# Performance work log

Measured on AMD Instinct MI355X. Metric: run time of the kernel, lower is better.

The kernel has to match this reference:

```python
import jax, jax.numpy as jnp
import numpy as np

D_MODEL = 1024
N_HEADS = 16
D_HEAD = D_MODEL // N_HEADS
MAX_K_LEN = 1024
SYNTH_HIDDEN = 1024
B, TQ, TK = 2, 1024, 1024
CAUSAL = True


def setup_inputs() -> dict:
    key = jax.random.key(0)
    ks = jax.random.split(key, 12)
    s = 1.0 / np.sqrt(D_MODEL)
    inp = {
        "x_q": jax.random.normal(ks[0], (B, TQ, D_MODEL), jnp.float32),
        "x_kv": jax.random.normal(ks[1], (B, TK, D_MODEL), jnp.float32),
        "key_padding_mask": jnp.ones((B, TK), jnp.int32),
        # projection weights stored [in, out] (equivalent to torch Linear)
        "Wq": jax.random.normal(ks[2], (D_MODEL, D_MODEL), jnp.float32) * s,
        "bq": jnp.zeros((D_MODEL,), jnp.float32),
        "Wk": jax.random.normal(ks[3], (D_MODEL, D_MODEL), jnp.float32) * s,
        "bk": jnp.zeros((D_MODEL,), jnp.float32),
        "Wv": jax.random.normal(ks[4], (D_MODEL, D_MODEL), jnp.float32) * s,
        "bv": jnp.zeros((D_MODEL,), jnp.float32),
        "Wo": jax.random.normal(ks[5], (D_MODEL, D_MODEL), jnp.float32) * s,
        "bo": jnp.zeros((D_MODEL,), jnp.float32),
        # synthesizer MLP: d_model -> synth_hidden -> n_heads*max_k_len
        "Ws1": jax.random.normal(ks[6], (D_MODEL, SYNTH_HIDDEN), jnp.float32) * s,
        "bs1": jnp.zeros((SYNTH_HIDDEN,), jnp.float32),
        "Ws2": jax.random.normal(ks[7], (SYNTH_HIDDEN, N_HEADS * MAX_K_LEN), jnp.float32) * (1.0 / np.sqrt(SYNTH_HIDDEN)),
        "bs2": jnp.zeros((N_HEADS * MAX_K_LEN,), jnp.float32),
        # gate logits init at log(0.5/0.5) = 0 -> sigmoid = 0.5
        "gate": jnp.zeros((N_HEADS,), jnp.float32),
    }
    return inp


def _attention(x_q, x_kv, key_padding_mask, Wq, bq, Wk, bk, Wv, bv, Wo, bo,
               Ws1, bs1, Ws2, bs2, gate):
    B_, Tq, _ = x_q.shape
    Tk = x_kv.shape[1]
    scale = D_HEAD ** -0.5

    def shape_heads(x):  # [B,T,D] -> [B,H,T,dh]
        return x.reshape(B_, -1, N_HEADS, D_HEAD).transpose(0, 2, 1, 3)

    Q = shape_heads(x_q @ Wq + bq)
    K = shape_heads(x_kv @ Wk + bk)
    V = shape_heads(x_kv @ Wv + bv)

    vanilla = jnp.einsum("bhqd,bhkd->bhqk", Q, K) * scale

    # dense synthesizer: MLP(x_q) -> [B,Tq,H,max_k_len] -> [B,H,Tq,Tk]
    h = jax.nn.gelu(x_q @ Ws1 + bs1, approximate=False)
    S = (h @ Ws2 + bs2).reshape(B_, Tq, N_HEADS, MAX_K_LEN)
    synth = S.transpose(0, 2, 1, 3)[:, :, :, :Tk]

    g = jax.nn.sigmoid(gate).reshape(1, N_HEADS, 1, 1)
    logits = (1.0 - g) * vanilla + g * synth

    # key padding mask: 1 = keep, 0 = pad
    keep = (key_padding_mask > 0).reshape(B_, 1, 1, Tk)
    logits = jnp.where(keep, logits, -jnp.inf)
    if CAUSAL:
        causal_mask = jnp.tril(jnp.ones((Tq, Tk), bool))  # keep lower triangle
        logits = jnp.where(causal_mask, logits, -jnp.inf)

    attn = jax.nn.softmax(logits, axis=-1)
    ctx = jnp.einsum("bhqk,bhkd->bhqd", attn, V)
    out = ctx.transpose(0, 2, 1, 3).reshape(B_, Tq, D_MODEL)
    return out @ Wo + bo


def reference(x_q, x_kv, key_padding_mask, Wq, bq, Wk, bk, Wv, bv, Wo, bo,
              Ws1, bs1, Ws2, bs2, gate):
    return _attention(x_q, x_kv, key_padding_mask, Wq, bq, Wk, bk, Wv, bv,
                      Wo, bo, Ws1, bs1, Ws2, bs2, gate)
```

## Files before the change

kernel.cpp:

```cpp
#include <hip/hip_runtime.h>
#include <hip/hip_bf16.h>

#define D_MODEL 1024
#define N_HEADS 16
#define MAX_K_LEN 1024
#define B_SZ 2
#define TQ 1024
#define TK 1024
#define M_ROWS 2048
#define NKL 16384

using bf16x8 = __attribute__((ext_vector_type(8))) short;
using f32x4  = __attribute__((ext_vector_type(4))) float;
using u16x8  = __attribute__((ext_vector_type(8))) unsigned short;

__device__ __forceinline__ unsigned short f2b(float f) {
    unsigned u = __float_as_uint(f);
    u = (u + 0x7FFFu + ((u >> 16) & 1u)) >> 16;
    return (unsigned short)u;
}
__device__ __forceinline__ float b2f(unsigned short u) {
    return __uint_as_float(((unsigned)u) << 16);
}

__device__ __forceinline__ void async_cp16(void* lds, const void* g) {
    __builtin_amdgcn_global_load_lds(
        (__attribute__((address_space(1))) void*)(void*)g,
        (__attribute__((address_space(3))) void*)lds, 16, 0, 0);
}

__device__ __forceinline__ int xrow(int row) {
    return (row & 7) ^ (((row >> 3) & 3) << 1);
}

__device__ __forceinline__ void ptile128_core(
    const unsigned short* __restrict__ A, const unsigned short* __restrict__ Wt,
    const float* __restrict__ bias, unsigned short* __restrict__ C,
    int N, int m0g, int n0g, int act, const float* __restrict__ gate,
    unsigned short* lds)
{
    constexpr int NT = 32;
    const int tid = threadIdx.x;
    const int lane = tid & 63;
    const int fr = lane & 15, rg = lane >> 4;
    const int w = tid >> 6;
    const int wr = w >> 1, wc = w & 1;

    const int sr = tid >> 2;
    const int sc = ((tid & 3) ^ ((sr >> 1) & 3)) * 8;
    const unsigned short* gA = A  + (size_t)(m0g + sr) * 1024 + sc;
    const unsigned short* gB = Wt + (size_t)(n0g + sr) * 1024 + sc;

    auto stage = [&](int t) {
        unsigned short* bufA = lds + (t % 3) * 8192;
        unsigned short* bufB = bufA + 4096;
        const int k0 = t * 32;
        async_cp16(bufA + tid*8,        gA + k0);
        async_cp16(bufA + 2048 + tid*8, gA + (size_t)64*1024 + k0);
        async_cp16(bufB + tid*8,        gB + k0);
        async_cp16(bufB + 2048 + tid*8, gB + (size_t)64*1024 + k0);
    };

    f32x4 acc[4][4];
#pragma unroll
    for (int i = 0; i < 4; ++i)
#pragma unroll
        for (int j = 0; j < 4; ++j) { f32x4 z = {0.f,0.f,0.f,0.f}; acc[i][j] = z; }

    const int fko = (rg ^ ((fr >> 1) & 3)) * 8;

    stage(0); stage(1);
    asm volatile("s_waitcnt vmcnt(4)" ::: "memory");
    __builtin_amdgcn_s_barrier();
    __builtin_amdgcn_sched_barrier(0);

    for (int t = 0; t < NT; ++t) {
        const unsigned short* bufA = lds + (t % 3) * 8192;
        const unsigned short* bufB = bufA + 4096;

        bf16x8 afr[4], bfr[4];
#pragma unroll
        for (int mi = 0; mi < 4; ++mi)
            afr[mi] = *(const bf16x8*)(bufA + (wr*64 + mi*16 + fr)*32 + fko);
#pragma unroll
        for (int ni = 0; ni < 4; ++ni)
            bfr[ni] = *(const bf16x8*)(bufB + (wc*64 + ni*16 + fr)*32 + fko);
        if (t + 2 < NT) stage(t + 2);

        __builtin_amdgcn_s_setprio(1);
#pragma unroll
        for (int mi = 0; mi < 4; ++mi)
#pragma unroll
            for (int ni = 0; ni < 4; ++ni)
                acc[mi][ni] = __builtin_amdgcn_mfma_f32_16x16x32_bf16(
                    afr[mi], bfr[ni], acc[mi][ni], 0, 0, 0);
        __builtin_amdgcn_s_setprio(0);

        if (t < NT - 2)       asm volatile("s_waitcnt vmcnt(4)" ::: "memory");
        else if (t == NT - 2) asm volatile("s_waitcnt vmcnt(0)" ::: "memory");
        __builtin_amdgcn_s_barrier();
        __builtin_amdgcn_sched_barrier(0);
    }

    float qs = 1.f;
    if (act == 2) {
        const float gg = 1.f / (1.f + __expf(-gate[(n0g + wc*64) >> 6]));
        qs = (1.f - gg) * 0.125f;
    }

    unsigned short* scr = lds + w * 1024;
    float bv[4];
#pragma unroll
    for (int ni = 0; ni < 4; ++ni) bv[ni] = bias[n0g + wc*64 + ni*16 + fr];
    const int ro = lane >> 3;
    const int co = (lane & 7) * 8;
#pragma unroll
    for (int mi = 0; mi < 4; ++mi) {
#pragma unroll
        for (int ni = 0; ni < 4; ++ni)
#pragma unroll
            for (int r = 0; r < 4; ++r) {
                float c = acc[mi][ni][r] + bv[ni];
                if (act == 1) c = 0.5f * c * (1.f + erff(c * 0.70710678118654752f));
                else if (act == 2) c *= qs;
                scr[(rg*4 + r)*64 + ni*16 + fr] = f2b(c);
            }
#pragma unroll
        for (int p = 0; p < 2; ++p) {
            const int row = p*8 + ro;
            const u16x8 v = *(const u16x8*)(scr + row*64 + co);
            *(u16x8*)(C + (size_t)(m0g + wr*64 + mi*16 + row) * N + n0g + wc*64 + co) = v;
        }
    }
}

struct QkvhArgs {
    const unsigned short* A[4];
    const unsigned short* W[4];
    const float* bias[4];
    void* out[4];
    const float* gate;
};

__global__ __launch_bounds__(256, 3) void gemm_qkvh_p(QkvhArgs args) {
    __shared__ __align__(16) unsigned short lds[24576];
    const int z = blockIdx.z;
    const int m0 = (blockIdx.x >> 3) * 128;
    const int n0 = (blockIdx.x & 7) * 128;
    const int act = (z == 3) ? 1 : ((z == 0) ? 2 : 0);
    ptile128_core(args.A[z], args.W[z], args.bias[z],
                  (unsigned short*)args.out[z], D_MODEL, m0, n0, act, args.gate, lds);
}

__global__ __launch_bounds__(256, 3) void gemm_logits_p(
    const unsigned short* __restrict__ A, const unsigned short* __restrict__ Wt,
    const float* __restrict__ bias, unsigned short* __restrict__ C,
    const unsigned short* __restrict__ Qpre, const unsigned short* __restrict__ Kb,
    const int* __restrict__ kpm)
{
    __shared__ __align__(16) unsigned short lds[24576];
    constexpr int NT = 34;
    const int bid = blockIdx.x;
    const int xcd = bid & 7;
    const int i = bid >> 3;
    const int hi = (i >= 72) ? 1 : 0;
    const int head = xcd * 2 + hi;
    const int j = i - hi * 72;
    int kq, idx;
    if (j < 16)      { kq = 0; idx = j; }
    else if (j < 30) { kq = 1; idx = j - 16; }
    else if (j < 42) { kq = 2; idx = j - 30; }
    else if (j < 52) { kq = 3; idx = j - 42; }
    else if (j < 60) { kq = 4; idx = j - 52; }
    else if (j < 66) { kq = 5; idx = j - 60; }
    else if (j < 70) { kq = 6; idx = j - 66; }
    else             { kq = 7; idx = j - 70; }
    const int b = idx & 1;
    const int rq = kq + (idx >> 1);
    const int m0g = (b * 8 + rq) * 128;
    const int n0g = (head * 8 + kq) * 128;

    const int tid = threadIdx.x;
    const int lane = tid & 63;
    const int fr = lane & 15, rg = lane >> 4;
    const int w = tid >> 6;
    const int wr = w >> 1, wc = w & 1;

    const int sr = tid >> 2;
    const int sc = ((tid & 3) ^ ((sr >> 1) & 3)) * 8;
    const unsigned short* gA = A  + (size_t)(m0g + sr) * 1024 + sc;
    const unsigned short* gB = Wt + (size_t)(n0g + sr) * 1024 + sc;
    const int q0 = rq * 128, k0a = kq * 128;
    const unsigned short* gA2 = Qpre + (size_t)(b*TQ + q0 + sr) * 1024 + head*64 + sc;
    const unsigned short* gB2 = Kb   + (size_t)(b*TK + k0a + sr) * 1024 + head*64 + sc;

    auto stageQK = [&](int t) {
        unsigned short* bufA = lds + (t % 3) * 8192;
        unsigned short* bufB = bufA + 4096;
        const int k0 = t * 32;
        async_cp16(bufA + tid*8,        gA2 + k0);
        async_cp16(bufA + 2048 + tid*8, gA2 + (size_t)64*1024 + k0);
        async_cp16(bufB + tid*8,        gB2 + k0);
        async_cp16(bufB + 2048 + tid*8, gB2 + (size_t)64*1024 + k0);
    };
    auto stageS = [&](int t) {
        unsigned short* bufA = lds + (t % 3) * 8192;
        unsigned short* bufB = bufA + 4096;
        const int k0 = (t - 2) * 32;
        async_cp16(bufA + tid*8,        gA + k0);
        async_cp16(bufA + 2048 + tid*8, gA + (size_t)64*1024 + k0);
        async_cp16(bufB + tid*8,        gB + k0);
        async_cp16(bufB + 2048 + tid*8, gB + (size_t)64*1024 + k0);
    };

    f32x4 acc[4][4];
#pragma unroll
    for (int ii = 0; ii < 4; ++ii)
#pragma unroll
        for (int jj = 0; jj < 4; ++jj) { f32x4 z = {0.f,0.f,0.f,0.f}; acc[ii][jj] = z; }

    const int fko = (rg ^ ((fr >> 1) & 3)) * 8;

    stageQK(0); stageQK(1);
    asm volatile("s_waitcnt vmcnt(4)" ::: "memory");
    __builtin_amdgcn_s_barrier();
    __builtin_amdgcn_sched_barrier(0);

    for (int t = 0; t < NT; ++t) {
        const unsigned short* bufA = lds + (t % 3) * 8192;
        const unsigned short* bufB = bufA + 4096;

        bf16x8 afr[4], bfr[4];
#pragma unroll
        for (int mi = 0; mi < 4; ++mi)
            afr[mi] = *(const bf16x8*)(bufA + (wr*64 + mi*16 + fr)*32 + fko);
#pragma unroll
        for (int ni = 0; ni < 4; ++ni)
            bfr[ni] = *(const bf16x8*)(bufB + (wc*64 + ni*16 + fr)*32 + fko);
        if (t + 2 < NT) stageS(t + 2);

        __builtin_amdgcn_s_setprio(1);
#pragma unroll
        for (int mi = 0; mi < 4; ++mi)
#pragma unroll
            for (int ni = 0; ni < 4; ++ni)
                acc[mi][ni] = __builtin_amdgcn_mfma_f32_16x16x32_bf16(
                    afr[mi], bfr[ni], acc[mi][ni], 0, 0, 0);
        __builtin_amdgcn_s_setprio(0);

        if (t < NT - 2)       asm volatile("s_waitcnt vmcnt(4)" ::: "memory");
        else if (t == NT - 2) asm volatile("s_waitcnt vmcnt(0)" ::: "memory");
        __builtin_amdgcn_s_barrier();
        __builtin_amdgcn_sched_barrier(0);
    }

    unsigned short* scr = lds + w * 1024;
    float bv[4];
    int kv[4];
#pragma unroll
    for (int ni = 0; ni < 4; ++ni) {
        const int colx = n0g + wc*64 + ni*16 + fr;
        bv[ni] = bias[colx];
        kv[ni] = kpm[b * TK + (colx & 1023)];
    }
    const int ro = lane >> 3;
    const int co = (lane & 7) * 8;
#pragma unroll
    for (int mi = 0; mi < 4; ++mi) {
#pragma unroll
        for (int ni = 0; ni < 4; ++ni) {
            const int k_idx = (n0g + wc*64 + ni*16 + fr) & 1023;
#pragma unroll
            for (int r = 0; r < 4; ++r) {
                const int q_idx = (m0g + wr*64 + mi*16 + rg*4 + r) & 1023;
                const bool ok = (kv[ni] > 0) && (k_idx <= q_idx);
                scr[(rg*4 + r)*64 + ni*16 + fr] =
                    ok ? f2b(acc[mi][ni][r] + bv[ni]) : (unsigned short)0xFF80u;
            }
        }
#pragma unroll
        for (int p = 0; p < 2; ++p) {
            const int row = p*8 + ro;
            const u16x8 v = *(const u16x8*)(scr + row*64 + co);
            *(u16x8*)(C + (size_t)(m0g + wr*64 + mi*16 + row) * NKL + n0g + wc*64 + co) = v;
        }
    }
}

__global__ __launch_bounds__(256, 3) void gemm_out_p(
    const unsigned short* __restrict__ A, const unsigned short* __restrict__ Wt,
    const float* __restrict__ bias, float* __restrict__ C)
{
    __shared__ __align__(16) unsigned short lds[24576];
    constexpr int NT = 32;
    const int m0g = blockIdx.y * 128;
    const int n0g = blockIdx.x * 128;

    const int tid = threadIdx.x;
    const int lane = tid & 63;
    const int fr = lane & 15, rg = lane >> 4;
    const int w = tid >> 6;
    const int wr = w >> 1, wc = w & 1;

    const int sr = tid >> 2;
    const int sc = ((tid & 3) ^ ((sr >> 1) & 3)) * 8;
    const unsigned short* gA = A  + (size_t)(m0g + sr) * 1024 + sc;
    const unsigned short* gB = Wt + (size_t)(n0g + sr) * 1024 + sc;

    auto stage = [&](int t) {
        unsigned short* bufA = lds + (t % 3) * 8192;
        unsigned short* bufB = bufA + 4096;
        const int k0 = t * 32;
        async_cp16(bufA + tid*8,        gA + k0);
        async_cp16(bufA + 2048 + tid*8, gA + (size_t)64*1024 + k0);
        async_cp16(bufB + tid*8,        gB + k0);
        async_cp16(bufB + 2048 + tid*8, gB + (size_t)64*1024 + k0);
    };

    f32x4 acc[4][4];
#pragma unroll
    for (int i = 0; i < 4; ++i)
#pragma unroll
        for (int j = 0; j < 4; ++j) { f32x4 z = {0.f,0.f,0.f,0.f}; acc[i][j] = z; }

    const int fko = (rg ^ ((fr >> 1) & 3)) * 8;

    stage(0); stage(1);
    asm volatile("s_waitcnt vmcnt(4)" ::: "memory");
    __builtin_amdgcn_s_barrier();
    __builtin_amdgcn_sched_barrier(0);

    for (int t = 0; t < NT; ++t) {
        const unsigned short* bufA = lds + (t % 3) * 8192;
        const unsigned short* bufB = bufA + 4096;

        bf16x8 afr[4], bfr[4];
#pragma unroll
        for (int mi = 0; mi < 4; ++mi)
            afr[mi] = *(const bf16x8*)(bufA + (wr*64 + mi*16 + fr)*32 + fko);
#pragma unroll
        for (int ni = 0; ni < 4; ++ni)
            bfr[ni] = *(const bf16x8*)(bufB + (wc*64 + ni*16 + fr)*32 + fko);
        if (t + 2 < NT) stage(t + 2);

        __builtin_amdgcn_s_setprio(1);
#pragma unroll
        for (int mi = 0; mi < 4; ++mi)
#pragma unroll
            for (int ni = 0; ni < 4; ++ni)
                acc[mi][ni] = __builtin_amdgcn_mfma_f32_16x16x32_bf16(
                    afr[mi], bfr[ni], acc[mi][ni], 0, 0, 0);
        __builtin_amdgcn_s_setprio(0);

        if (t < NT - 2)       asm volatile("s_waitcnt vmcnt(4)" ::: "memory");
        else if (t == NT - 2) asm volatile("s_waitcnt vmcnt(0)" ::: "memory");
        __builtin_amdgcn_s_barrier();
        __builtin_amdgcn_sched_barrier(0);
    }

#pragma unroll
    for (int ni = 0; ni < 4; ++ni) {
        const int colx = n0g + wc*64 + ni*16 + fr;
        const float bvv = bias[colx];
#pragma unroll
        for (int mi = 0; mi < 4; ++mi)
#pragma unroll
            for (int r = 0; r < 4; ++r) {
                const int row = m0g + wr*64 + mi*16 + rg*4 + r;
                C[(size_t)row * D_MODEL + colx] = acc[mi][ni][r] + bvv;
            }
    }
}

struct PrepArgs {
    const float* xq; const float* xkv;
    unsigned short* xq_b; unsigned short* xkv_b;
    const float* W[6]; unsigned short* Wt[6]; int Nw[6];
    const float* bs2; float* bs2g; const float* gate;
};

__global__ __launch_bounds__(256) void prep_all(PrepArgs p) {
    __shared__ float T[32][33];
    int id = blockIdx.x;
    if (id < 4096) {
        const float* src = (id < 2048) ? p.xq : p.xkv;
        unsigned short* dst = (id < 2048) ? p.xq_b : p.xkv_b;
        const int i = (id & 2047) * 256 + threadIdx.x;
        const float4 v = ((const float4*)src)[i];
        ushort4 o; o.x = f2b(v.x); o.y = f2b(v.y); o.z = f2b(v.z); o.w = f2b(v.w);
        ((ushort4*)dst)[i] = o;
        return;
    }
    if (id >= 25600) {
        const int i = (id - 25600) * 256 + threadIdx.x;
        const float gg = 1.f / (1.f + __expf(-p.gate[i >> 10]));
        p.bs2g[i] = gg * p.bs2[i];
        return;
    }
    id -= 4096;
    int seg, lb;
    if (id < 5120) { seg = id >> 10; lb = id & 1023; }
    else           { seg = 5;        lb = id - 5120; }
    const int N = p.Nw[seg];
    const int nx = N >> 5;
    const int bx = lb % nx, by = lb / nx;
    const int n0 = bx * 32, k0 = by * 32;
    const float* W = p.W[seg];
    unsigned short* Wt = p.Wt[seg];
    float gs = 1.f;
    if (seg == 5) gs = 1.f / (1.f + __expf(-p.gate[n0 >> 10]));
    const int r = threadIdx.x >> 3, c = (threadIdx.x & 7) * 4;
    const float4 v = *(const float4*)&W[(size_t)(k0 + r) * N + n0 + c];
    T[r][c] = v.x; T[r][c+1] = v.y; T[r][c+2] = v.z; T[r][c+3] = v.w;
    __syncthreads();
    ushort4 o;
    o.x = f2b(T[c][r] * gs); o.y = f2b(T[c+1][r] * gs);
    o.z = f2b(T[c+2][r] * gs); o.w = f2b(T[c+3][r] * gs);
    *(ushort4*)&Wt[(size_t)(n0 + r) * D_MODEL + k0 + c] = o;
}

__global__ __launch_bounds__(256) void rowstat(
    const unsigned short* __restrict__ Lb,
    float* __restrict__ Ms, float* __restrict__ Is)
{
    const int id = blockIdx.x * 4 + (threadIdx.x >> 6);
    const int lane = threadIdx.x & 63;
    const int row = id >> 4;
    const int h = id & 15;
    const int q = row & 1023;
    const unsigned short* src = Lb + (size_t)row * NKL + h * MAX_K_LEN + lane;
    const int nj = (q >> 6) + 1;

    float vals[16];
    float vmax = -INFINITY;
#pragma unroll
    for (int j = 0; j < 16; ++j) {
        if (j < nj) {
            vals[j] = b2f(src[j * 64]);
            vmax = fmaxf(vmax, vals[j]);
        } else vals[j] = -INFINITY;
    }
#pragma unroll
    for (int o = 32; o; o >>= 1) vmax = fmaxf(vmax, __shfl_xor(vmax, o));

    float s = 0.f;
#pragma unroll
    for (int j = 0; j < 16; ++j)
        if (j < nj && vals[j] != -INFINITY) s += __expf(vals[j] - vmax);
#pragma unroll
    for (int o = 32; o; o >>= 1) s += __shfl_xor(s, o);

    if (lane == 0) {
        if (vmax == -INFINITY) { Ms[row * 16 + h] = 0.f; Is[row * 16 + h] = 0.f; }
        else { Ms[row * 16 + h] = vmax; Is[row * 16 + h] = 1.f / s; }
    }
}

__global__ __launch_bounds__(256) void attn_pv(
    const unsigned short* __restrict__ Lb, const unsigned short* __restrict__ Vb,
    const float* __restrict__ Ms, const float* __restrict__ Is,
    unsigned short* __restrict__ ctx)
{
    const int bx = blockIdx.x;
    const int q1 = bx >> 1;
    const int qt = (bx & 1) ? q1 : (15 - q1);
    const int h = blockIdx.y, b = blockIdx.z;
    const int tid = threadIdx.x;
    const int lane = tid & 63;
    const int w = tid >> 6;
    const int col = lane & 15, rg = lane >> 4;
    const int q0g = qt * 64;

    __shared__ __align__(16) unsigned short Ls[2][64*64];
    __shared__ __align__(16) unsigned short Vt[2][64*64];

    const int srr = tid >> 3, scp = tid & 7;
    auto issueL = [&](int kt, int buf) {
        const unsigned short* gs = Lb + ((size_t)(b*TQ + q0g)) * NKL + h*MAX_K_LEN + kt*64;
        async_cp16(Ls[buf] + tid*8,        gs + (size_t)srr*NKL + (scp ^ xrow(srr))*8);
        async_cp16(Ls[buf] + 2048 + tid*8, gs + (size_t)(srr+32)*NKL + (scp ^ xrow(srr+32))*8);
    };
    const int vk = tid >> 2, vdc = (tid & 3) * 16;
    const int vkc = vk >> 3, vke = vk & 7;
    u16x8 vr0, vr1;
    auto loadV = [&](int kt) {
        const unsigned short* gv = Vb + ((size_t)(b*TK + kt*64 + vk)) * D_MODEL + h*64 + vdc;
        vr0 = *(const u16x8*)gv;
        vr1 = *(const u16x8*)(gv + 8);
    };
    auto writeV = [&](int buf) {
#pragma unroll
        for (int j = 0; j < 8; ++j) {
            const int d0 = vdc + j, d1 = vdc + 8 + j;
            Vt[buf][d0*64 + (vkc ^ xrow(d0))*8 + vke] = vr0[j];
            Vt[buf][d1*64 + (vkc ^ xrow(d1))*8 + vke] = vr1[j];
        }
    };

    const int qrow = q0g + w*16 + col;
    const float m_row  = Ms[((size_t)(b*1024 + qrow)) * 16 + h];
    const float inv_row = Is[((size_t)(b*1024 + qrow)) * 16 + h];

    issueL(0, 0);
    loadV(0);
    writeV(0);
    __syncthreads();

    f32x4 octx[4];
#pragma unroll
    for (int n = 0; n < 4; ++n) { f32x4 z = {0.f,0.f,0.f,0.f}; octx[n] = z; }

    for (int kt = 0; kt <= qt; ++kt) {
        const int cur = kt & 1;
        if (kt < qt) { issueL(kt + 1, cur ^ 1); loadV(kt + 1); }

#pragma unroll
        for (int s = 0; s < 2; ++s) {
            const int lrow = w*16 + col;
            const bf16x8 lf = *(const bf16x8*)(Ls[cur] + lrow*64 + ((s*4 + rg) ^ xrow(lrow))*8);
            bf16x8 pa;
#pragma unroll
            for (int jj = 0; jj < 8; ++jj) {
                const float p = __expf(b2f((unsigned short)lf[jj]) - m_row) * inv_row;
                pa[jj] = (short)f2b(p);
            }
#pragma unroll
            for (int n = 0; n < 4; ++n) {
                const int d = n*16 + col;
                const bf16x8 vv = *(const bf16x8*)(Vt[cur] + d*64 + ((s*4 + rg) ^ xrow(d))*8);
                octx[n] = __builtin_amdgcn_mfma_f32_16x16x32_bf16(pa, vv, octx[n], 0, 0, 0);
            }
        }

        if (kt < qt) writeV(cur ^ 1);
        __syncthreads();
    }

#pragma unroll
    for (int n = 0; n < 4; ++n)
#pragma unroll
        for (int r = 0; r < 4; ++r) {
            const size_t row = (size_t)(b*TQ + q0g + w*16 + rg*4 + r);
            ctx[row*D_MODEL + h*64 + n*16 + col] = f2b(octx[n][r]);
        }
}

extern "C" void kernel_launch(void* const* d_in, const int* in_sizes, int n_in,
                              void* d_out, int out_size, void* d_ws, size_t ws_size,
                              hipStream_t stream) {
    const float* x_q  = (const float*)d_in[0];
    const float* x_kv = (const float*)d_in[1];
    const int*   kpm  = (const int*)d_in[2];
    const float* Wq  = (const float*)d_in[3];  const float* bq  = (const float*)d_in[4];
    const float* Wk  = (const float*)d_in[5];  const float* bk  = (const float*)d_in[6];
    const float* Wv  = (const float*)d_in[7];  const float* bv  = (const float*)d_in[8];
    const float* Wo  = (const float*)d_in[9];  const float* bo  = (const float*)d_in[10];
    const float* Ws1 = (const float*)d_in[11]; const float* bs1 = (const float*)d_in[12];
    const float* Ws2 = (const float*)d_in[13]; const float* bs2 = (const float*)d_in[14];
    const float* gate = (const float*)d_in[15];

    char* ws = (char*)d_ws;
    const size_t MB = 1024ull * 1024ull;
    unsigned short* Sb    = (unsigned short*)ws;
    unsigned short* xq_b  = (unsigned short*)ws;
    unsigned short* xkv_b = (unsigned short*)(ws + 4*MB);
    size_t off = 64*MB;
    unsigned short* Wq_t  = (unsigned short*)(ws + off); off += 2*MB;
    unsigned short* Wk_t  = (unsigned short*)(ws + off); off += 2*MB;
    unsigned short* Wv_t  = (unsigned short*)(ws + off); off += 2*MB;
    unsigned short* Wo_t  = (unsigned short*)(ws + off); off += 2*MB;
    unsigned short* Ws1_t = (unsigned short*)(ws + off); off += 2*MB;
    unsigned short* Ws2_t = (unsigned short*)(ws + off); off += 32*MB;
    unsigned short* Qb    = (unsigned short*)(ws + off); off += 4*MB;
    unsigned short* Kb    = (unsigned short*)(ws + off); off += 4*MB;
    unsigned short* Vb    = (unsigned short*)(ws + off); off += 4*MB;
    unsigned short* hb    = (unsigned short*)(ws + off); off += 4*MB;
    unsigned short* ctxb  = (unsigned short*)(ws + off); off += 4*MB;
    float* bs2g           = (float*)(ws + off); off += 64*1024;
    float* Ms             = (float*)(ws + off); off += 128*1024;
    float* Is             = (float*)(ws + off); off += 128*1024;

    dim3 blk(256);

    PrepArgs pa;
    pa.xq = x_q; pa.xkv = x_kv; pa.xq_b = xq_b; pa.xkv_b = xkv_b;
    pa.W[0] = Wq;  pa.Wt[0] = Wq_t;  pa.Nw[0] = D_MODEL;
    pa.W[1] = Wk;  pa.Wt[1] = Wk_t;  pa.Nw[1] = D_MODEL;
    pa.W[2] = Wv;  pa.Wt[2] = Wv_t;  pa.Nw[2] = D_MODEL;
    pa.W[3] = Wo;  pa.Wt[3] = Wo_t;  pa.Nw[3] = D_MODEL;
    pa.W[4] = Ws1; pa.Wt[4] = Ws1_t; pa.Nw[4] = D_MODEL;
    pa.W[5] = Ws2; pa.Wt[5] = Ws2_t; pa.Nw[5] = NKL;
    pa.bs2 = bs2; pa.bs2g = bs2g; pa.gate = gate;
    prep_all<<<dim3(25664), blk, 0, stream>>>(pa);

    QkvhArgs qa;
    qa.A[0] = xq_b;  qa.W[0] = Wq_t;  qa.bias[0] = bq;  qa.out[0] = Qb;
    qa.A[1] = xkv_b; qa.W[1] = Wk_t;  qa.bias[1] = bk;  qa.out[1] = Kb;
    qa.A[2] = xkv_b; qa.W[2] = Wv_t;  qa.bias[2] = bv;  qa.out[2] = Vb;
    qa.A[3] = xq_b;  qa.W[3] = Ws1_t; qa.bias[3] = bs1; qa.out[3] = hb;
    qa.gate = gate;
    gemm_qkvh_p<<<dim3(128, 1, 4), dim3(256), 0, stream>>>(qa);

    gemm_logits_p<<<dim3(1152), dim3(256), 0, stream>>>(hb, Ws2_t, bs2g, Sb, Qb, Kb, kpm);

    rowstat<<<dim3(8192), blk, 0, stream>>>(Sb, Ms, Is);

    attn_pv<<<dim3(TQ/64, N_HEADS, B_SZ), blk, 0, stream>>>(Sb, Vb, Ms, Is, ctxb);

    gemm_out_p<<<dim3(8, 16), dim3(256), 0, stream>>>(ctxb, Wo_t, bo, (float*)d_out);
}
```

Baseline: 170.4 us.

## Split attention PV kernel along key dimension and add combine pass

Splits each query tile's causal key range into two halves handled by separate blocks, doubling the grid of the attn_pv kernel, and writes bf16 partial contexts into a scratch buffer that reuses the Ws2_t workspace. A new attn_combine kernel sums the two partials and writes the ctx layout. The aim is more parallelism and better load balance on a many-CU GPU, at the cost of an extra launch, extra memory traffic, and an additional bf16 rounding of the partial sums. It also adds a minimum-occupancy hint to the launch bounds.

New measurement: 172.1 us. Within noise of the previous version (+1.0%).

```diff
diff --git a/kernel.cpp b/kernel.cpp
--- a/kernel.cpp
+++ b/kernel.cpp
@@ -456,20 +456,37 @@
     }
 }
 
-__global__ __launch_bounds__(256) void attn_pv(
+__global__ __launch_bounds__(256, 4) void attn_pv(
     const unsigned short* __restrict__ Lb, const unsigned short* __restrict__ Vb,
     const float* __restrict__ Ms, const float* __restrict__ Is,
-    unsigned short* __restrict__ ctx)
+    unsigned short* __restrict__ Op)
 {
     const int bx = blockIdx.x;
-    const int q1 = bx >> 1;
-    const int qt = (bx & 1) ? q1 : (15 - q1);
+    const int s = bx & 1;
+    const int u = bx >> 1;
+    const int q1 = u >> 1;
+    const int qt = (u & 1) ? q1 : (15 - q1);
     const int h = blockIdx.y, b = blockIdx.z;
     const int tid = threadIdx.x;
     const int lane = tid & 63;
     const int w = tid >> 6;
     const int col = lane & 15, rg = lane >> 4;
     const int q0g = qt * 64;
+
+    const int nt  = qt + 1;
+    const int nt0 = (nt + 1) >> 1;
+    const int ktb = s ? nt0 : 0;
+    const int kte = s ? nt : nt0;
+
+    unsigned short* obase = Op + (((size_t)s * B_SZ + b) * N_HEADS + h) * (TQ * 64);
+
+    if (ktb >= kte) {
+        const int zr = tid >> 2, zc = (tid & 3) * 16;
+        u16x8 z = {0,0,0,0,0,0,0,0};
+        *(u16x8*)(obase + (size_t)(q0g + zr) * 64 + zc)     = z;
+        *(u16x8*)(obase + (size_t)(q0g + zr) * 64 + zc + 8) = z;
+        return;
+    }
 
     __shared__ __align__(16) unsigned short Ls[2][64*64];
     __shared__ __align__(16) unsigned short Vt[2][64*64];
@@ -498,11 +515,11 @@
     };
 
     const int qrow = q0g + w*16 + col;
-    const float m_row  = Ms[((size_t)(b*1024 + qrow)) * 16 + h];
+    const float m_row   = Ms[((size_t)(b*1024 + qrow)) * 16 + h];
     const float inv_row = Is[((size_t)(b*1024 + qrow)) * 16 + h];
 
-    issueL(0, 0);
-    loadV(0);
+    issueL(ktb, 0);
+    loadV(ktb);
     writeV(0);
     __syncthreads();
 
@@ -510,14 +527,14 @@
 #pragma unroll
     for (int n = 0; n < 4; ++n) { f32x4 z = {0.f,0.f,0.f,0.f}; octx[n] = z; }
 
-    for (int kt = 0; kt <= qt; ++kt) {
-        const int cur = kt & 1;
-        if (kt < qt) { issueL(kt + 1, cur ^ 1); loadV(kt + 1); }
-
-#pragma unroll
-        for (int s = 0; s < 2; ++s) {
+    for (int kt = ktb; kt < kte; ++kt) {
+        const int cur = (kt - ktb) & 1;
+        if (kt + 1 < kte) { issueL(kt + 1, cur ^ 1); loadV(kt + 1); }
+
+#pragma unroll
+        for (int sl = 0; sl < 2; ++sl) {
             const int lrow = w*16 + col;
-            const bf16x8 lf = *(const bf16x8*)(Ls[cur] + lrow*64 + ((s*4 + rg) ^ xrow(lrow))*8);
+            const bf16x8 lf = *(const bf16x8*)(Ls[cur] + lrow*64 + ((sl*4 + rg) ^ xrow(lrow))*8);
             bf16x8 pa;
 #pragma unroll
             for (int jj = 0; jj < 8; ++jj) {
@@ -527,12 +544,12 @@
 #pragma unroll
             for (int n = 0; n < 4; ++n) {
                 const int d = n*16 + col;
-                const bf16x8 vv = *(const bf16x8*)(Vt[cur] + d*64 + ((s*4 + rg) ^ xrow(d))*8);
+                const bf16x8 vv = *(const bf16x8*)(Vt[cur] + d*64 + ((sl*4 + rg) ^ xrow(d))*8);
                 octx[n] = __builtin_amdgcn_mfma_f32_16x16x32_bf16(pa, vv, octx[n], 0, 0, 0);
             }
         }
 
-        if (kt < qt) writeV(cur ^ 1);
+        if (kt + 1 < kte) writeV(cur ^ 1);
         __syncthreads();
     }
 
@@ -540,9 +557,21 @@
     for (int n = 0; n < 4; ++n)
 #pragma unroll
         for (int r = 0; r < 4; ++r) {
-            const size_t row = (size_t)(b*TQ + q0g + w*16 + rg*4 + r);
-            ctx[row*D_MODEL + h*64 + n*16 + col] = f2b(octx[n][r]);
+            const int q = q0g + w*16 + rg*4 + r;
+            obase[(size_t)q * 64 + n*16 + col] = f2b(octx[n][r]);
         }
+}
+
+__global__ __launch_bounds__(256) void attn_combine(
+    const unsigned short* __restrict__ Op, unsigned short* __restrict__ ctx)
+{
+    const int id = blockIdx.x * 4 + (threadIdx.x >> 6);
+    const int d = threadIdx.x & 63;
+    const int b = id >> 14, h = (id >> 10) & 15, q = id & 1023;
+    const size_t i0 = (((size_t)b * N_HEADS + h) * TQ + q) * 64 + d;
+    const size_t i1 = i0 + (size_t)B_SZ * N_HEADS * TQ * 64;
+    const float o = b2f(Op[i0]) + b2f(Op[i1]);
+    ctx[((size_t)(b * TQ + q)) * D_MODEL + h * 64 + d] = f2b(o);
 }
 
 extern "C" void kernel_launch(void* const* d_in, const int* in_sizes, int n_in,
@@ -580,6 +609,8 @@
     float* Ms             = (float*)(ws + off); off += 128*1024;
     float* Is             = (float*)(ws + off); off += 128*1024;
 
+    unsigned short* Op = Ws2_t;
+
     dim3 blk(256);
 
     PrepArgs pa;
@@ -605,7 +636,8 @@
 
     rowstat<<<dim3(8192), blk, 0, stream>>>(Sb, Ms, Is);
 
-    attn_pv<<<dim3(TQ/64, N_HEADS, B_SZ), blk, 0, stream>>>(Sb, Vb, Ms, Is, ctxb);
+    attn_pv<<<dim3(32, N_HEADS, B_SZ), blk, 0, stream>>>(Sb, Vb, Ms, Is, Op);
+    attn_combine<<<dim3(8192), blk, 0, stream>>>(Op, ctxb);
 
     gemm_out_p<<<dim3(8, 16), dim3(256), 0, stream>>>(ctxb, Wo_t, bo, (float*)d_out);
 }
```
